# Kernel optimization log

Measured on AMD Instinct MI355X. Metric: run time of the kernel, lower is better.

The kernel has to match this reference:

```python
import jax, jax.numpy as jnp
import numpy as np

D = 127          # feature dim d
TD = D + 1       # token_dim = d + 1 = 128
H = D            # hidden_dim defaults to d
L = 2            # num_layers
EPS = 1e-6       # block eps
LN_EPS = 1e-5    # torch LayerNorm default


def _layernorm(x, w, b):
    m = jnp.mean(x, axis=-1, keepdims=True)
    v = jnp.mean(jnp.square(x - m), axis=-1, keepdims=True)
    return (x - m) * jax.lax.rsqrt(v + LN_EPS) * w + b


def _phi(x):
    return jax.nn.elu(x) + 1.0


def _gla_block(tokens, wq, wk, wv, wg_w, wg_b, wo, l1w, l1b, l2w, l2b):
    # tokens: (B, T, TD)
    x = _layernorm(tokens, l1w, l1b)
    Q = x @ wq.T                      # (B,T,H)
    K = x @ wk.T                      # (B,T,H)
    V = x @ wv.T                      # (B,T,TD)
    G = jax.nn.sigmoid(x @ wg_w.T + wg_b)
    Vg = V * G
    Qp = _phi(Q)
    Kp = _phi(K)
    # causal linear attention via cumulative outer-product state
    kv = jnp.einsum('bth,btm->bthm', Kp, Vg)   # (B,T,H,TD)
    S_kv = jnp.cumsum(kv, axis=1)
    S_k = jnp.cumsum(Kp, axis=1)
    numerator = jnp.einsum('bth,bthm->btm', Qp, S_kv)   # (B,T,TD)
    denom = jnp.maximum(jnp.einsum('bth,bth->bt', Qp, S_k), EPS)
    attn_out = numerator / denom[..., None]
    out = tokens + (attn_out @ wo.T) * 0.1
    return _layernorm(out, l2w, l2b)


def setup_inputs() -> dict:
    key = jax.random.key(0)
    ks = jax.random.split(key, 16)
    B, N = 2, 4095
    s = 0.02  # small xavier-ish gain used by the module
    inp = {
        'xs': jax.random.normal(ks[0], (B, N, D), jnp.float32),
        'ys': jax.random.normal(ks[1], (B, N), jnp.float32),
        'query_x': jax.random.normal(ks[2], (B, 1, D), jnp.float32),
        'Wq': jax.random.normal(ks[3], (L, H, TD), jnp.float32) * s,
        'Wk': jax.random.normal(ks[4], (L, H, TD), jnp.float32) * s,
        'Wv': jax.random.normal(ks[5], (L, TD, TD), jnp.float32) * s,
        'Wg_w': jax.random.normal(ks[6], (L, TD, TD), jnp.float32) * s,
        'Wg_b': jnp.zeros((L, TD), jnp.float32),
        'Wo': jax.random.normal(ks[7], (L, TD, TD), jnp.float32) * s,
        'ln1_w': jnp.ones((L, TD), jnp.float32),
        'ln1_b': jnp.zeros((L, TD), jnp.float32),
        'ln2_w': jnp.ones((L, TD), jnp.float32),
        'ln2_b': jnp.zeros((L, TD), jnp.float32),
        'pred_w': jax.random.normal(ks[8], (1, TD), jnp.float32) * 0.1,
    }
    return inp


def reference(xs, ys, query_x, Wq, Wk, Wv, Wg_w, Wg_b, Wo,
              ln1_w, ln1_b, ln2_w, ln2_b, pred_w):
    B = xs.shape[0]
    train_tokens = jnp.concatenate([xs, ys[..., None]], axis=-1)       # (B,N,TD)
    query_token = jnp.concatenate(
        [query_x, jnp.zeros((B, 1, 1), xs.dtype)], axis=-1)            # (B,1,TD)
    tokens = jnp.concatenate([train_tokens, query_token], axis=1)      # (B,T,TD)
    for l in range(L):
        tokens = _gla_block(tokens, Wq[l], Wk[l], Wv[l], Wg_w[l], Wg_b[l],
                            Wo[l], ln1_w[l], ln1_b[l], ln2_w[l], ln2_b[l])
    y_pred = tokens[:, -1, :] @ pred_w.T   # (B,1)
    return y_pred[:, 0]
```

## Files before the change

kernel.cpp:

```cpp
#include <hip/hip_runtime.h>
#include <hip/hip_bf16.h>

#define TT 4096
#define NCH 32
#define BB 2

__device__ float g_tok[(size_t)BB*TT*128];
__device__ float g_Qp [(size_t)BB*TT*128];
__device__ float g_Kp [(size_t)BB*TT*128];
__device__ float g_Vg [(size_t)BB*TT*128];
__device__ float g_Pv [(size_t)BB*TT*128];
__device__ float g_Pg [(size_t)BB*TT*128];
__device__ float g_Ssum[(size_t)BB*NCH*16384];
__device__ float g_Spre[(size_t)BB*NCH*16384];
__device__ float g_Sk [(size_t)BB*NCH*128];
__device__ float g_Skp[(size_t)BB*NCH*128];

__device__ __forceinline__ float phi_f(float x){ return x > 0.f ? x + 1.f : __expf(x); }
__device__ __forceinline__ float sigm_f(float x){ return 1.f/(1.f+__expf(-x)); }

__global__ __launch_bounds__(256) void k0_build(const float* __restrict__ xs,
                                                const float* __restrict__ ys,
                                                const float* __restrict__ qx){
  long e = (long)blockIdx.x * 256 + threadIdx.x;
  int col = (int)(e & 127);
  long r = e >> 7;
  int t = (int)(r & (TT-1));
  int b = (int)(r >> 12);
  float v;
  if (t < TT-1) {
    v = (col < 127) ? xs[((long)b*(TT-1) + t)*127 + col] : ys[(long)b*(TT-1) + t];
  } else {
    v = (col < 127) ? qx[(long)b*127 + col] : 0.f;
  }
  g_tok[e] = v;
}

__global__ __launch_bounds__(256) void k1b_gemm(
    const float* __restrict__ Wq, const float* __restrict__ Wk,
    const float* __restrict__ Wv, const float* __restrict__ Wg,
    const float* __restrict__ lnw, const float* __restrict__ lnb)
{
  __shared__ float xl[128*132];
  __shared__ float wt[128*132];
  int tid = threadIdx.x;
  int mat = blockIdx.x & 3;
  long row0 = (long)(blockIdx.x >> 2) * 128;
  const float* W = (mat==0) ? Wq : (mat==1) ? Wk : (mat==2) ? Wv : Wg;
  bool isQK = (mat < 2);
  for (int i=0;i<16;i++){
    int ts = (tid & 31) + 32*(i & 3);
    int hc = (tid >> 5) + 8*(i >> 2);
    int wr = isQK ? (ts < 127 ? ts : 126) : ts;
    float4 v = *(const float4*)(W + (long)wr*128 + hc*4);
    wt[(hc*4+0)*132+ts] = v.x;
    wt[(hc*4+1)*132+ts] = v.y;
    wt[(hc*4+2)*132+ts] = v.z;
    wt[(hc*4+3)*132+ts] = v.w;
  }
  {
    int row = tid >> 1, half = tid & 1;
    const float* src = g_tok + (row0 + row)*128 + half*64;
    float s1 = 0.f, s2 = 0.f;
    for (int u=0; u<16; u++){
      float4 v = *(const float4*)(src + u*4);
      s1 += v.x+v.y+v.z+v.w;
      s2 += v.x*v.x+v.y*v.y+v.z*v.z+v.w*v.w;
      *(float4*)&xl[row*132 + half*64 + u*4] = v;
    }
    s1 += __shfl_xor(s1, 1); s2 += __shfl_xor(s2, 1);
    float mean = s1*(1.f/128.f);
    float var  = s2*(1.f/128.f) - mean*mean;
    float rstd = rsqrtf(var + 1e-5f);
    for (int u=0; u<16; u++){
      int cc = half*64 + u*4;
      float4 v  = *(float4*)&xl[row*132 + cc];
      float4 w4 = *(const float4*)(lnw + cc);
      float4 b4 = *(const float4*)(lnb + cc);
      v.x = (v.x-mean)*rstd*w4.x + b4.x;
      v.y = (v.y-mean)*rstd*w4.y + b4.y;
      v.z = (v.z-mean)*rstd*w4.z + b4.z;
      v.w = (v.w-mean)*rstd*w4.w + b4.w;
      *(float4*)&xl[row*132 + cc] = v;
    }
  }
  __syncthreads();
  int g = tid >> 4, c = tid & 15;
  float acc[8][8];
  #pragma unroll
  for (int i=0;i<8;i++)
    #pragma unroll
    for (int j=0;j<8;j++) acc[i][j]=0.f;
  for (int k=0;k<128;k++){
    float xr[8];
    #pragma unroll
    for (int i=0;i<8;i++) xr[i] = xl[(g+16*i)*132 + k];
    float4 wa = *(const float4*)&wt[k*132 + c*4];
    float4 wb = *(const float4*)&wt[k*132 + 64 + c*4];
    float wc[8] = {wa.x,wa.y,wa.z,wa.w,wb.x,wb.y,wb.z,wb.w};
    #pragma unroll
    for (int i=0;i<8;i++)
      #pragma unroll
      for (int j=0;j<8;j++)
        acc[i][j] += xr[i]*wc[j];
  }
  if (isQK){
    float* dst = (mat==0) ? g_Qp : g_Kp;
    #pragma unroll
    for (int i=0;i<8;i++){
      long rr = row0 + g + 16*i;
      float v0[4], v1[4];
      #pragma unroll
      for (int j=0;j<4;j++) v0[j] = phi_f(acc[i][j]);
      #pragma unroll
      for (int j=0;j<4;j++){
        int col = 64 + c*4 + j;
        v1[j] = (col < 127) ? phi_f(acc[i][4+j]) : 0.f;
      }
      *(float4*)(dst + rr*128 + c*4)      = make_float4(v0[0],v0[1],v0[2],v0[3]);
      *(float4*)(dst + rr*128 + 64 + c*4) = make_float4(v1[0],v1[1],v1[2],v1[3]);
    }
  } else {
    float* dst = (mat==2) ? g_Pv : g_Pg;
    #pragma unroll
    for (int i=0;i<8;i++){
      long rr = row0 + g + 16*i;
      *(float4*)(dst + rr*128 + c*4)      = make_float4(acc[i][0],acc[i][1],acc[i][2],acc[i][3]);
      *(float4*)(dst + rr*128 + 64 + c*4) = make_float4(acc[i][4],acc[i][5],acc[i][6],acc[i][7]);
    }
  }
}

__global__ __launch_bounds__(256) void k1c_vg(const float* __restrict__ Wgb){
  long e = ((long)blockIdx.x*256 + threadIdx.x) * 4;
  int j = (int)(e & 127);
  float4 pv = *(const float4*)(g_Pv + e);
  float4 pg = *(const float4*)(g_Pg + e);
  float4 gb = *(const float4*)(Wgb + j);
  float4 o;
  o.x = pv.x * sigm_f(pg.x + gb.x);
  o.y = pv.y * sigm_f(pg.y + gb.y);
  o.z = pv.z * sigm_f(pg.z + gb.z);
  o.w = pv.w * sigm_f(pg.w + gb.w);
  *(float4*)(g_Vg + e) = o;
}

__global__ __launch_bounds__(256) void k2_chunksum()
{
  __shared__ float vgs[16][128];
  __shared__ float kps[16][32];
  int tid = threadIdx.x;
  int ht = blockIdx.x & 3;
  int c  = (blockIdx.x >> 2) & 31;
  int b  = blockIdx.x >> 7;
  int hl = tid >> 3, mg = tid & 7, m0 = mg << 4;
  int h  = ht*32 + hl;
  float acc[16];
  #pragma unroll
  for (int i=0;i<16;i++) acc[i]=0.f;
  float sk = 0.f;
  long base = ((long)b*TT + c*128)*128;
  for (int tb=0; tb<8; tb++){
    __syncthreads();
    { int e = tid*8; int ts = e >> 7; int cc = e & 127;
      const float* s = g_Vg + base + (long)(tb*16+ts)*128 + cc;
      *(float4*)&vgs[ts][cc]   = *(const float4*)s;
      *(float4*)&vgs[ts][cc+4] = *(const float4*)(s+4); }
    { int e = tid*2; int ts = e >> 5; int hh = e & 31;
      const float* s = g_Kp + base + (long)(tb*16+ts)*128 + ht*32 + hh;
      kps[ts][hh] = s[0]; kps[ts][hh+1] = s[1]; }
    __syncthreads();
    for (int ts=0; ts<16; ts++){
      float kp = kps[ts][hl];
      sk += kp;
      #pragma unroll
      for (int i=0;i<16;i++) acc[i] += kp * vgs[ts][m0+i];
    }
  }
  long so = (((long)b*NCH + c)*128 + h)*128 + m0;
  #pragma unroll
  for (int i=0;i<16;i+=4)
    *(float4*)(g_Ssum + so + i) = make_float4(acc[i],acc[i+1],acc[i+2],acc[i+3]);
  if (mg==0) g_Sk[((long)b*NCH + c)*128 + h] = sk;
}

__global__ __launch_bounds__(256) void k3_scan()
{
  if (blockIdx.x < 32){
    int gid = blockIdx.x*256 + threadIdx.x;
    int b  = gid >> 12;
    int e4 = gid & 4095;
    long base = ((long)b*NCH)*16384 + (long)e4*4;
    float4 v[NCH];
    #pragma unroll
    for (int c=0;c<NCH;c++)
      v[c] = *(const float4*)(g_Ssum + base + (long)c*16384);
    float4 run = make_float4(0.f,0.f,0.f,0.f);
    #pragma unroll
    for (int c=0;c<NCH;c++){
      *(float4*)(g_Spre + base + (long)c*16384) = run;
      run.x += v[c].x; run.y += v[c].y; run.z += v[c].z; run.w += v[c].w;
    }
  } else {
    int b = threadIdx.x >> 7, h = threadIdx.x & 127;
    long base = ((long)b*NCH)*128 + h;
    float v[NCH];
    #pragma unroll
    for (int c=0;c<NCH;c++) v[c] = g_Sk[base + c*128];
    float run = 0.f;
    #pragma unroll
    for (int c=0;c<NCH;c++){
      g_Skp[base + c*128] = run;
      run += v[c];
    }
  }
}

__global__ __launch_bounds__(256) void k4_fused(
    const float* __restrict__ Wo,
    const float* __restrict__ ln2w, const float* __restrict__ ln2b)
{
  __shared__ float spl[128*132];
  __shared__ float ktl[128*132];
  __shared__ float bufb[32*133];
  __shared__ float skl[128];
  int tid = threadIdx.x;
  int rq = blockIdx.x & 3;
  int c  = (blockIdx.x >> 2) & 31;
  int b  = blockIdx.x >> 7;
  int r0 = rq*32;
  long cbase = ((long)b*TT + c*128)*128;
  long sbase = ((long)b*NCH + c)*16384;

  for (int i=0;i<16;i++){
    int e = i*1024 + tid*4;
    int h = e >> 7, n = e & 127;
    *(float4*)&spl[h*132+n] = *(const float4*)(g_Spre + sbase + e);
  }
  if (tid < 128) skl[tid] = g_Skp[((long)b*NCH + c)*128 + tid];
  for (int i=0;i<4;i++){
    int e = i*1024 + tid*4;
    int row = e >> 7, cc = e & 127;
    *(float4*)&bufb[row*133+cc] = *(const float4*)(g_Qp + cbase + (long)(r0+row)*128 + cc);
  }
  for (int i=0;i<16;i++){
    int ts = (tid & 31) + 32*(i & 3);
    int hc = (tid >> 5) + 8*(i >> 2);
    float4 v = *(const float4*)(g_Kp + cbase + (long)ts*128 + hc*4);
    ktl[(hc*4+0)*132 + ts] = v.x;
    ktl[(hc*4+1)*132 + ts] = v.y;
    ktl[(hc*4+2)*132 + ts] = v.z;
    ktl[(hc*4+3)*132 + ts] = v.w;
  }
  __syncthreads();

  int rg = tid >> 5, cs = tid & 31;
  int n0 = cs*4;
  float acc2[4][4], a[4][4];
  #pragma unroll
  for (int r=0;r<4;r++)
    #pragma unroll
    for (int j=0;j<4;j++){ acc2[r][j]=0.f; a[r][j]=0.f; }
  float den[4] = {0.f,0.f,0.f,0.f};
  for (int h=0;h<128;h++){
    float sv = skl[h];
    float4 s4 = *(const float4*)&spl[h*132 + n0];
    float4 k4 = *(const float4*)&ktl[h*132 + n0];
    #pragma unroll
    for (int r=0;r<4;r++){
      float qv = bufb[(4*rg+r)*133 + h];
      den[r] += qv*sv;
      acc2[r][0]+=qv*s4.x; acc2[r][1]+=qv*s4.y; acc2[r][2]+=qv*s4.z; acc2[r][3]+=qv*s4.w;
      a[r][0]+=qv*k4.x; a[r][1]+=qv*k4.y; a[r][2]+=qv*k4.z; a[r][3]+=qv*k4.w;
    }
  }
  float inv[4];
  #pragma unroll
  for (int r=0;r<4;r++){
    int tq = r0 + 4*rg + r;
    float dena = 0.f;
    #pragma unroll
    for (int j=0;j<4;j++){
      if (n0 + j > tq) a[r][j] = 0.f;
      dena += a[r][j];
    }
    dena += __shfl_xor(dena, 1);
    dena += __shfl_xor(dena, 2);
    dena += __shfl_xor(dena, 4);
    dena += __shfl_xor(dena, 8);
    dena += __shfl_xor(dena, 16);
    inv[r] = 1.f / fmaxf(den[r] + dena, 1e-6f);
  }
  __syncthreads();
  #pragma unroll
  for (int r=0;r<4;r++)
    *(float4*)&bufb[(4*rg+r)*133 + n0] = make_float4(a[r][0],a[r][1],a[r][2],a[r][3]);
  for (int i=0;i<16;i++){
    int e = i*1024 + tid*4;
    *(float4*)&ktl[e] = *(const float4*)(g_Vg + cbase + e);
  }
  __syncthreads();
  for (int ts=0; ts<128; ts++){
    float4 v4 = *(const float4*)&ktl[ts*128 + n0];
    #pragma unroll
    for (int r=0;r<4;r++){
      float av = bufb[(4*rg+r)*133 + ts];
      acc2[r][0]+=av*v4.x; acc2[r][1]+=av*v4.y; acc2[r][2]+=av*v4.z; acc2[r][3]+=av*v4.w;
    }
  }
  __syncthreads();
  #pragma unroll
  for (int r=0;r<4;r++)
    *(float4*)&bufb[(4*rg+r)*133 + n0] =
      make_float4(acc2[r][0]*inv[r],acc2[r][1]*inv[r],acc2[r][2]*inv[r],acc2[r][3]*inv[r]);
  for (int i=0;i<16;i++){
    int n  = (tid & 31) + 32*(i & 3);
    int mc = (tid >> 5) + 8*(i >> 2);
    float4 v = *(const float4*)(Wo + (long)n*128 + mc*4);
    ktl[(mc*4+0)*132 + n] = v.x;
    ktl[(mc*4+1)*132 + n] = v.y;
    ktl[(mc*4+2)*132 + n] = v.z;
    ktl[(mc*4+3)*132 + n] = v.w;
  }
  __syncthreads();
  float s[4][4];
  #pragma unroll
  for (int r=0;r<4;r++)
    #pragma unroll
    for (int j=0;j<4;j++) s[r][j]=0.f;
  for (int m=0;m<128;m++){
    float4 w4 = *(const float4*)&ktl[m*132 + n0];
    #pragma unroll
    for (int r=0;r<4;r++){
      float av = bufb[(4*rg+r)*133 + m];
      s[r][0]+=av*w4.x; s[r][1]+=av*w4.y; s[r][2]+=av*w4.z; s[r][3]+=av*w4.w;
    }
  }
  float4 lw = *(const float4*)(ln2w+n0);
  float4 lb = *(const float4*)(ln2b+n0);
  #pragma unroll
  for (int r=0;r<4;r++){
    long trow = (long)b*TT + c*128 + r0 + 4*rg + r;
    float4 t4 = *(const float4*)(g_tok + trow*128 + n0);
    float o0 = t4.x + 0.1f*s[r][0];
    float o1 = t4.y + 0.1f*s[r][1];
    float o2 = t4.z + 0.1f*s[r][2];
    float o3 = t4.w + 0.1f*s[r][3];
    float s1 = o0+o1+o2+o3;
    float s2 = o0*o0+o1*o1+o2*o2+o3*o3;
    s1 += __shfl_xor(s1,1);  s2 += __shfl_xor(s2,1);
    s1 += __shfl_xor(s1,2);  s2 += __shfl_xor(s2,2);
    s1 += __shfl_xor(s1,4);  s2 += __shfl_xor(s2,4);
    s1 += __shfl_xor(s1,8);  s2 += __shfl_xor(s2,8);
    s1 += __shfl_xor(s1,16); s2 += __shfl_xor(s2,16);
    float mean = s1*(1.f/128.f);
    float var  = s2*(1.f/128.f) - mean*mean;
    float rstd = rsqrtf(var + 1e-5f);
    float4 o;
    o.x = (o0-mean)*rstd*lw.x + lb.x;
    o.y = (o1-mean)*rstd*lw.y + lb.y;
    o.z = (o2-mean)*rstd*lw.z + lb.z;
    o.w = (o3-mean)*rstd*lw.w + lb.w;
    *(float4*)(g_tok + trow*128 + n0) = o;
  }
}

__global__ __launch_bounds__(128) void k5_pred(const float* __restrict__ pw,
                                               float* __restrict__ out){
  __shared__ float red[2];
  int b = blockIdx.x, tid = threadIdx.x;
  float v = g_tok[((long)b*TT + TT-1)*128 + tid] * pw[tid];
  #pragma unroll
  for (int off=1; off<64; off<<=1) v += __shfl_xor(v, off);
  if ((tid & 63) == 0) red[tid>>6] = v;
  __syncthreads();
  if (tid==0) out[b] = red[0] + red[1];
}

extern "C" void kernel_launch(void* const* d_in, const int* in_sizes, int n_in,
                              void* d_out, int out_size, void* d_ws, size_t ws_size,
                              hipStream_t stream)
{
  (void)in_sizes; (void)n_in; (void)out_size; (void)d_ws; (void)ws_size;
  const float* xs   = (const float*)d_in[0];
  const float* ys   = (const float*)d_in[1];
  const float* qx   = (const float*)d_in[2];
  const float* Wq   = (const float*)d_in[3];
  const float* Wk   = (const float*)d_in[4];
  const float* Wv   = (const float*)d_in[5];
  const float* Wgw  = (const float*)d_in[6];
  const float* Wgb  = (const float*)d_in[7];
  const float* Wo   = (const float*)d_in[8];
  const float* ln1w = (const float*)d_in[9];
  const float* ln1b = (const float*)d_in[10];
  const float* ln2w = (const float*)d_in[11];
  const float* ln2b = (const float*)d_in[12];
  const float* predw= (const float*)d_in[13];

  k0_build<<<4096, 256, 0, stream>>>(xs, ys, qx);

  for (int l=0; l<2; l++){
    const float* Wq_l  = Wq  + (size_t)l*127*128;
    const float* Wk_l  = Wk  + (size_t)l*127*128;
    const float* Wv_l  = Wv  + (size_t)l*128*128;
    const float* Wgw_l = Wgw + (size_t)l*128*128;
    const float* Wgb_l = Wgb + (size_t)l*128;
    const float* Wo_l  = Wo  + (size_t)l*128*128;
    const float* l1w = ln1w + (size_t)l*128;
    const float* l1b = ln1b + (size_t)l*128;
    const float* l2w = ln2w + (size_t)l*128;
    const float* l2b = ln2b + (size_t)l*128;

    k1b_gemm<<<256, 256, 0, stream>>>(Wq_l, Wk_l, Wv_l, Wgw_l, l1w, l1b);
    k1c_vg<<<1024, 256, 0, stream>>>(Wgb_l);
    k2_chunksum<<<256, 256, 0, stream>>>();
    k3_scan<<<33, 256, 0, stream>>>();
    k4_fused<<<256, 256, 0, stream>>>(Wo_l, l2w, l2b);
  }
  k5_pred<<<BB, 128, 0, stream>>>(predw, (float*)d_out);
}
```

Measured before the change: 248.5 us.

## Halve shared-memory footprint in GEMM and fused attention kernels for occupancy

Both the projection GEMM kernel and the fused attention/output kernel now stage their K-dimension operands in two 64-wide halves through a single smaller LDS buffer. The fused kernel also reads the prefix state straight from global memory instead of staging it in LDS. Launch bounds request 2 and 3 blocks per CU so more workgroups can be resident. The cost is extra barriers, a serialized second load phase in each kernel, and uncached global reads of the state matrix inside the inner loop.

```diff
diff --git a/kernel.cpp b/kernel.cpp
--- a/kernel.cpp
+++ b/kernel.cpp
@@ -36,65 +36,105 @@
   g_tok[e] = v;
 }
 
-__global__ __launch_bounds__(256) void k1b_gemm(
+__global__ __launch_bounds__(256, 2) void k1b_gemm(
     const float* __restrict__ Wq, const float* __restrict__ Wk,
     const float* __restrict__ Wv, const float* __restrict__ Wg,
     const float* __restrict__ lnw, const float* __restrict__ lnb)
 {
-  __shared__ float xl[128*132];
-  __shared__ float wt[128*132];
+  __shared__ float xh[128*68];
+  __shared__ float wt[64*132];
+  __shared__ float mr[256];
   int tid = threadIdx.x;
   int mat = blockIdx.x & 3;
   long row0 = (long)(blockIdx.x >> 2) * 128;
   const float* W = (mat==0) ? Wq : (mat==1) ? Wk : (mat==2) ? Wv : Wg;
   bool isQK = (mat < 2);
-  for (int i=0;i<16;i++){
-    int ts = (tid & 31) + 32*(i & 3);
-    int hc = (tid >> 5) + 8*(i >> 2);
-    int wr = isQK ? (ts < 127 ? ts : 126) : ts;
-    float4 v = *(const float4*)(W + (long)wr*128 + hc*4);
-    wt[(hc*4+0)*132+ts] = v.x;
-    wt[(hc*4+1)*132+ts] = v.y;
-    wt[(hc*4+2)*132+ts] = v.z;
-    wt[(hc*4+3)*132+ts] = v.w;
-  }
+  int row = tid >> 1, half = tid & 1;
+  const float* src = g_tok + (row0 + row)*128 + half*64;
   {
-    int row = tid >> 1, half = tid & 1;
-    const float* src = g_tok + (row0 + row)*128 + half*64;
     float s1 = 0.f, s2 = 0.f;
     for (int u=0; u<16; u++){
       float4 v = *(const float4*)(src + u*4);
       s1 += v.x+v.y+v.z+v.w;
       s2 += v.x*v.x+v.y*v.y+v.z*v.z+v.w*v.w;
-      *(float4*)&xl[row*132 + half*64 + u*4] = v;
     }
     s1 += __shfl_xor(s1, 1); s2 += __shfl_xor(s2, 1);
     float mean = s1*(1.f/128.f);
     float var  = s2*(1.f/128.f) - mean*mean;
     float rstd = rsqrtf(var + 1e-5f);
+    if (half == 0){
+      mr[row*2] = mean; mr[row*2+1] = rstd;
+      for (int u=0; u<16; u++){
+        float4 v  = *(const float4*)(src + u*4);
+        float4 w4 = *(const float4*)(lnw + u*4);
+        float4 b4 = *(const float4*)(lnb + u*4);
+        v.x = (v.x-mean)*rstd*w4.x + b4.x;
+        v.y = (v.y-mean)*rstd*w4.y + b4.y;
+        v.z = (v.z-mean)*rstd*w4.z + b4.z;
+        v.w = (v.w-mean)*rstd*w4.w + b4.w;
+        *(float4*)&xh[row*68 + u*4] = v;
+      }
+    }
+  }
+  for (int i=0;i<8;i++){
+    int ts  = (tid & 31) + 32*(i & 3);
+    int hcl = (tid >> 5) + 8*(i >> 2);
+    int wr = isQK ? (ts < 127 ? ts : 126) : ts;
+    float4 v = *(const float4*)(W + (long)wr*128 + hcl*4);
+    wt[(hcl*4+0)*132+ts] = v.x;
+    wt[(hcl*4+1)*132+ts] = v.y;
+    wt[(hcl*4+2)*132+ts] = v.z;
+    wt[(hcl*4+3)*132+ts] = v.w;
+  }
+  __syncthreads();
+  int g = tid >> 4, c = tid & 15;
+  float acc[8][8];
+  #pragma unroll
+  for (int i=0;i<8;i++)
+    #pragma unroll
+    for (int j=0;j<8;j++) acc[i][j]=0.f;
+  for (int k=0;k<64;k++){
+    float xr[8];
+    #pragma unroll
+    for (int i=0;i<8;i++) xr[i] = xh[(g+16*i)*68 + k];
+    float4 wa = *(const float4*)&wt[k*132 + c*4];
+    float4 wb = *(const float4*)&wt[k*132 + 64 + c*4];
+    float wc[8] = {wa.x,wa.y,wa.z,wa.w,wb.x,wb.y,wb.z,wb.w};
+    #pragma unroll
+    for (int i=0;i<8;i++)
+      #pragma unroll
+      for (int j=0;j<8;j++)
+        acc[i][j] += xr[i]*wc[j];
+  }
+  __syncthreads();
+  if (half == 1){
+    float mean = mr[row*2], rstd = mr[row*2+1];
     for (int u=0; u<16; u++){
-      int cc = half*64 + u*4;
-      float4 v  = *(float4*)&xl[row*132 + cc];
-      float4 w4 = *(const float4*)(lnw + cc);
-      float4 b4 = *(const float4*)(lnb + cc);
+      float4 v  = *(const float4*)(src + u*4);
+      float4 w4 = *(const float4*)(lnw + 64 + u*4);
+      float4 b4 = *(const float4*)(lnb + 64 + u*4);
       v.x = (v.x-mean)*rstd*w4.x + b4.x;
       v.y = (v.y-mean)*rstd*w4.y + b4.y;
       v.z = (v.z-mean)*rstd*w4.z + b4.z;
       v.w = (v.w-mean)*rstd*w4.w + b4.w;
-      *(float4*)&xl[row*132 + cc] = v;
-    }
-  }
-  __syncthreads();
-  int g = tid >> 4, c = tid & 15;
-  float acc[8][8];
-  #pragma unroll
-  for (int i=0;i<8;i++)
-    #pragma unroll
-    for (int j=0;j<8;j++) acc[i][j]=0.f;
-  for (int k=0;k<128;k++){
+      *(float4*)&xh[row*68 + u*4] = v;
+    }
+  }
+  for (int i=0;i<8;i++){
+    int ts  = (tid & 31) + 32*(i & 3);
+    int hcl = (tid >> 5) + 8*(i >> 2);
+    int wr = isQK ? (ts < 127 ? ts : 126) : ts;
+    float4 v = *(const float4*)(W + (long)wr*128 + 64 + hcl*4);
+    wt[(hcl*4+0)*132+ts] = v.x;
+    wt[(hcl*4+1)*132+ts] = v.y;
+    wt[(hcl*4+2)*132+ts] = v.z;
+    wt[(hcl*4+3)*132+ts] = v.w;
+  }
+  __syncthreads();
+  for (int k=0;k<64;k++){
     float xr[8];
     #pragma unroll
-    for (int i=0;i<8;i++) xr[i] = xl[(g+16*i)*132 + k];
+    for (int i=0;i<8;i++) xr[i] = xh[(g+16*i)*68 + k];
     float4 wa = *(const float4*)&wt[k*132 + c*4];
     float4 wb = *(const float4*)&wt[k*132 + 64 + c*4];
     float wc[8] = {wa.x,wa.y,wa.z,wa.w,wb.x,wb.y,wb.z,wb.w};
@@ -216,12 +256,11 @@
   }
 }
 
-__global__ __launch_bounds__(256) void k4_fused(
+__global__ __launch_bounds__(256, 3) void k4_fused(
     const float* __restrict__ Wo,
     const float* __restrict__ ln2w, const float* __restrict__ ln2b)
 {
-  __shared__ float spl[128*132];
-  __shared__ float ktl[128*132];
+  __shared__ float buf[64*132];
   __shared__ float bufb[32*133];
   __shared__ float skl[128];
   int tid = threadIdx.x;
@@ -230,27 +269,22 @@
   int b  = blockIdx.x >> 7;
   int r0 = rq*32;
   long cbase = ((long)b*TT + c*128)*128;
-  long sbase = ((long)b*NCH + c)*16384;
-
-  for (int i=0;i<16;i++){
-    int e = i*1024 + tid*4;
-    int h = e >> 7, n = e & 127;
-    *(float4*)&spl[h*132+n] = *(const float4*)(g_Spre + sbase + e);
-  }
-  if (tid < 128) skl[tid] = g_Skp[((long)b*NCH + c)*128 + tid];
+  const float* sp = g_Spre + ((long)b*NCH + c)*16384;
+
   for (int i=0;i<4;i++){
     int e = i*1024 + tid*4;
     int row = e >> 7, cc = e & 127;
     *(float4*)&bufb[row*133+cc] = *(const float4*)(g_Qp + cbase + (long)(r0+row)*128 + cc);
   }
-  for (int i=0;i<16;i++){
-    int ts = (tid & 31) + 32*(i & 3);
-    int hc = (tid >> 5) + 8*(i >> 2);
-    float4 v = *(const float4*)(g_Kp + cbase + (long)ts*128 + hc*4);
-    ktl[(hc*4+0)*132 + ts] = v.x;
-    ktl[(hc*4+1)*132 + ts] = v.y;
-    ktl[(hc*4+2)*132 + ts] = v.z;
-    ktl[(hc*4+3)*132 + ts] = v.w;
+  if (tid < 128) skl[tid] = g_Skp[((long)b*NCH + c)*128 + tid];
+  for (int i=0;i<8;i++){
+    int ts  = (tid & 31) + 32*(i & 3);
+    int hcl = (tid >> 5) + 8*(i >> 2);
+    float4 v = *(const float4*)(g_Kp + cbase + (long)ts*128 + hcl*4);
+    buf[(hcl*4+0)*132 + ts] = v.x;
+    buf[(hcl*4+1)*132 + ts] = v.y;
+    buf[(hcl*4+2)*132 + ts] = v.z;
+    buf[(hcl*4+3)*132 + ts] = v.w;
   }
   __syncthreads();
 
@@ -262,10 +296,33 @@
     #pragma unroll
     for (int j=0;j<4;j++){ acc2[r][j]=0.f; a[r][j]=0.f; }
   float den[4] = {0.f,0.f,0.f,0.f};
-  for (int h=0;h<128;h++){
+  for (int h=0;h<64;h++){
     float sv = skl[h];
-    float4 s4 = *(const float4*)&spl[h*132 + n0];
-    float4 k4 = *(const float4*)&ktl[h*132 + n0];
+    float4 s4 = *(const float4*)(sp + (long)h*128 + n0);
+    float4 k4 = *(const float4*)&buf[h*132 + n0];
+    #pragma unroll
+    for (int r=0;r<4;r++){
+      float qv = bufb[(4*rg+r)*133 + h];
+      den[r] += qv*sv;
+      acc2[r][0]+=qv*s4.x; acc2[r][1]+=qv*s4.y; acc2[r][2]+=qv*s4.z; acc2[r][3]+=qv*s4.w;
+      a[r][0]+=qv*k4.x; a[r][1]+=qv*k4.y; a[r][2]+=qv*k4.z; a[r][3]+=qv*k4.w;
+    }
+  }
+  __syncthreads();
+  for (int i=0;i<8;i++){
+    int ts  = (tid & 31) + 32*(i & 3);
+    int hcl = (tid >> 5) + 8*(i >> 2);
+    float4 v = *(const float4*)(g_Kp + cbase + (long)ts*128 + 64 + hcl*4);
+    buf[(hcl*4+0)*132 + ts] = v.x;
+    buf[(hcl*4+1)*132 + ts] = v.y;
+    buf[(hcl*4+2)*132 + ts] = v.z;
+    buf[(hcl*4+3)*132 + ts] = v.w;
+  }
+  __syncthreads();
+  for (int h=64;h<128;h++){
+    float sv = skl[h];
+    float4 s4 = *(const float4*)(sp + (long)h*128 + n0);
+    float4 k4 = *(const float4*)&buf[(h-64)*132 + n0];
     #pragma unroll
     for (int r=0;r<4;r++){
       float qv = bufb[(4*rg+r)*133 + h];
@@ -295,13 +352,13 @@
   #pragma unroll
   for (int r=0;r<4;r++)
     *(float4*)&bufb[(4*rg+r)*133 + n0] = make_float4(a[r][0],a[r][1],a[r][2],a[r][3]);
-  for (int i=0;i<16;i++){
+  for (int i=0;i<8;i++){
     int e = i*1024 + tid*4;
-    *(float4*)&ktl[e] = *(const float4*)(g_Vg + cbase + e);
-  }
-  __syncthreads();
-  for (int ts=0; ts<128; ts++){
-    float4 v4 = *(const float4*)&ktl[ts*128 + n0];
+    *(float4*)&buf[e] = *(const float4*)(g_Vg + cbase + e);
+  }
+  __syncthreads();
+  for (int ts=0; ts<64; ts++){
+    float4 v4 = *(const float4*)&buf[ts*128 + n0];
     #pragma unroll
     for (int r=0;r<4;r++){
       float av = bufb[(4*rg+r)*133 + ts];
@@ -309,18 +366,32 @@
     }
   }
   __syncthreads();
+  for (int i=0;i<8;i++){
+    int e = i*1024 + tid*4;
+    *(float4*)&buf[e] = *(const float4*)(g_Vg + cbase + 8192 + e);
+  }
+  __syncthreads();
+  for (int ts=64; ts<128; ts++){
+    float4 v4 = *(const float4*)&buf[(ts-64)*128 + n0];
+    #pragma unroll
+    for (int r=0;r<4;r++){
+      float av = bufb[(4*rg+r)*133 + ts];
+      acc2[r][0]+=av*v4.x; acc2[r][1]+=av*v4.y; acc2[r][2]+=av*v4.z; acc2[r][3]+=av*v4.w;
+    }
+  }
+  __syncthreads();
   #pragma unroll
   for (int r=0;r<4;r++)
     *(float4*)&bufb[(4*rg+r)*133 + n0] =
       make_float4(acc2[r][0]*inv[r],acc2[r][1]*inv[r],acc2[r][2]*inv[r],acc2[r][3]*inv[r]);
-  for (int i=0;i<16;i++){
-    int n  = (tid & 31) + 32*(i & 3);
-    int mc = (tid >> 5) + 8*(i >> 2);
-    float4 v = *(const float4*)(Wo + (long)n*128 + mc*4);
-    ktl[(mc*4+0)*132 + n] = v.x;
-    ktl[(mc*4+1)*132 + n] = v.y;
-    ktl[(mc*4+2)*132 + n] = v.z;
-    ktl[(mc*4+3)*132 + n] = v.w;
+  for (int i=0;i<8;i++){
+    int n   = (tid & 31) + 32*(i & 3);
+    int mcl = (tid >> 5) + 8*(i >> 2);
+    float4 v = *(const float4*)(Wo + (long)n*128 + mcl*4);
+    buf[(mcl*4+0)*132 + n] = v.x;
+    buf[(mcl*4+1)*132 + n] = v.y;
+    buf[(mcl*4+2)*132 + n] = v.z;
+    buf[(mcl*4+3)*132 + n] = v.w;
   }
   __syncthreads();
   float s[4][4];
@@ -328,8 +399,27 @@
   for (int r=0;r<4;r++)
     #pragma unroll
     for (int j=0;j<4;j++) s[r][j]=0.f;
-  for (int m=0;m<128;m++){
-    float4 w4 = *(const float4*)&ktl[m*132 + n0];
+  for (int m=0; m<64; m++){
+    float4 w4 = *(const float4*)&buf[m*132 + n0];
+    #pragma unroll
+    for (int r=0;r<4;r++){
+      float av = bufb[(4*rg+r)*133 + m];
+      s[r][0]+=av*w4.x; s[r][1]+=av*w4.y; s[r][2]+=av*w4.z; s[r][3]+=av*w4.w;
+    }
+  }
+  __syncthreads();
+  for (int i=0;i<8;i++){
+    int n   = (tid & 31) + 32*(i & 3);
+    int mcl = (tid >> 5) + 8*(i >> 2);
+    float4 v = *(const float4*)(Wo + (long)n*128 + 64 + mcl*4);
+    buf[(mcl*4+0)*132 + n] = v.x;
+    buf[(mcl*4+1)*132 + n] = v.y;
+    buf[(mcl*4+2)*132 + n] = v.z;
+    buf[(mcl*4+3)*132 + n] = v.w;
+  }
+  __syncthreads();
+  for (int m=64; m<128; m++){
+    float4 w4 = *(const float4*)&buf[(m-64)*132 + n0];
     #pragma unroll
     for (int r=0;r<4;r++){
       float av = bufb[(4*rg+r)*133 + m];
```

Result: no change. 248.9 us (+0.2%).
